# Optimization experiments

Hardware: AMD Instinct MI355X
Metric: run time of the kernel (lower is better)

The kernel has to match this reference:

```python
import jax, jax.numpy as jnp
import numpy as np
from jax import lax

B, T = 8192, 4096


def setup_inputs() -> dict:
    key = jax.random.key(0)
    kx, k1, k2, k3, k4 = jax.random.split(key, 5)
    # torch.nn.RNN default init: U(-1/sqrt(hidden), 1/sqrt(hidden)) = U(-1, 1) for hidden=1
    u = lambda k, shp: jax.random.uniform(k, shp, jnp.float32, -1.0, 1.0)
    return {
        "x": jax.random.normal(kx, (B, T, 1), jnp.float32),
        "w_ih": u(k1, (1, 1)),
        "w_hh": u(k2, (1, 1)),
        "b_ih": u(k3, (1,)),
        "b_hh": u(k4, (1,)),
    }


def reference(x, w_ih, w_hh, b_ih, b_hh):
    # Vanilla tanh RNN: h_t = tanh(x_t @ W_ih^T + b_ih + h_{t-1} @ W_hh^T + b_hh)
    # hidden=input=1, so all matmuls are scalar multiplies. Output is h at last step.
    a = w_ih[0, 0]
    b = w_hh[0, 0]
    c = b_ih[0] + b_hh[0]
    xT = jnp.swapaxes(x, 0, 1)  # [T, B, 1]

    def step(h, x_t):
        h_new = jnp.tanh(x_t * a + h * b + c)
        return h_new, None

    h0 = jnp.zeros((x.shape[0], 1), x.dtype)
    hT, _ = lax.scan(step, h0, xT)
    return hT  # [B, 1], equals rnn_output[:, -1]
```

## Files before the change

kernel.cpp:

```cpp
#include <hip/hip_runtime.h>


constexpr int T_LEN = 4096;
constexpr int NTHR  = 256;
constexpr int CH    = T_LEN / NTHR;
constexpr int NF4   = CH / 4;

typedef float fx4 __attribute__((ext_vector_type(4)));

__device__ __forceinline__ int swz(int s) { return s ^ ((s >> 2) & 7); }

#define STEP_PG(qv)                                                     \
    do {                                                                \
        float r_ = __builtin_amdgcn_rcpf(E + 1.0f);                     \
        P *= (fourb * r_) * (1.0f - r_);                                \
        E = __builtin_amdgcn_exp2f(fmaf(r_, nB4, (qv)));                \
    } while (0)

__global__ __launch_bounds__(NTHR)
void rnn_row_kernel(const float* __restrict__ x,
                    const float* __restrict__ w_ih,
                    const float* __restrict__ w_hh,
                    const float* __restrict__ b_ih,
                    const float* __restrict__ b_hh,
                    float* __restrict__ out) {
    __shared__ fx4 sm[T_LEN / 4];
    __shared__ float wP[4], wG[4];

    const int tid  = threadIdx.x;
    const int lane = tid & 63;
    const int wv   = tid >> 6;
    const int row  = blockIdx.x;

    const float a  = w_ih[0];
    const float bb = w_hh[0];
    const float cc = b_ih[0] + b_hh[0];

    const float L2E2  = 2.88539008177792681472f;
    const float A2    = a * L2E2;
    const float C2    = (bb + cc) * L2E2;
    const float nB4   = -(bb * L2E2 * 2.0f);
    const float fourb = 4.0f * bb;

    const fx4* xp = (const fx4*)(x + (size_t)row * T_LEN);
#pragma unroll
    for (int i = 0; i < 4; ++i) {
        int s = (wv << 8) + (i << 6) + lane;
        sm[swz(s)] = xp[s];
    }

    fx4 buf[NF4];
#pragma unroll
    for (int q = 0; q < NF4; ++q) buf[q] = sm[swz(tid * NF4 + q)];

    float E, P = 1.0f;
    {
        fx4 v = buf[0];
        float q0 = fmaf(v.x, A2, C2);
        float q1 = fmaf(v.y, A2, C2);
        float q2 = fmaf(v.z, A2, C2);
        float q3 = fmaf(v.w, A2, C2);
        E = __builtin_amdgcn_exp2f(fmaf(0.5f, nB4, q0));
        STEP_PG(q1); STEP_PG(q2); STEP_PG(q3);
    }
#pragma unroll
    for (int i = 1; i < NF4; ++i) {
        fx4 v = buf[i];
        float q0 = fmaf(v.x, A2, C2);
        float q1 = fmaf(v.y, A2, C2);
        float q2 = fmaf(v.z, A2, C2);
        float q3 = fmaf(v.w, A2, C2);
        STEP_PG(q0); STEP_PG(q1); STEP_PG(q2); STEP_PG(q3);
    }
    float r = __builtin_amdgcn_rcpf(E + 1.0f);
    float G = fmaf(-2.0f, r, 1.0f);
    P *= (fourb * r) * (1.0f - r);

#pragma unroll
    for (int d = 1; d < 64; d <<= 1) {
        float Pl = __shfl_up(P, d, 64);
        float Gl = __shfl_up(G, d, 64);
        if (lane >= d) {
            G = fmaf(P, Gl, G);
            P *= Pl;
        }
    }
    if (lane == 63) { wP[wv] = P; wG[wv] = G; }
    __syncthreads();

    if (tid == 0) {
        float h = wG[0];
        h = fmaf(wP[1], h, wG[1]);
        h = fmaf(wP[2], h, wG[2]);
        h = fmaf(wP[3], h, wG[3]);
        out[row] = h;
    }
}

extern "C" void kernel_launch(void* const* d_in, const int* in_sizes, int n_in,
                              void* d_out, int out_size, void* d_ws, size_t ws_size,
                              hipStream_t stream) {
    const float* x    = (const float*)d_in[0];
    const float* w_ih = (const float*)d_in[1];
    const float* w_hh = (const float*)d_in[2];
    const float* b_ih = (const float*)d_in[3];
    const float* b_hh = (const float*)d_in[4];
    float* out = (float*)d_out;

    const int B = out_size;
    dim3 grid(B), block(NTHR);
    rnn_row_kernel<<<grid, block, 0, stream>>>(x, w_ih, w_hh, b_ih, b_hh, out);
}
```

Before: 190.8 us.

## Process four rows per block with register prefetch of the next row

```diff
diff --git a/kernel.cpp b/kernel.cpp
--- a/kernel.cpp
+++ b/kernel.cpp
@@ -5,6 +5,7 @@
 constexpr int NTHR  = 256;
 constexpr int CH    = T_LEN / NTHR;
 constexpr int NF4   = CH / 4;
+constexpr int RPB   = 4;
 
 typedef float fx4 __attribute__((ext_vector_type(4)));
 
@@ -17,7 +18,7 @@
         E = __builtin_amdgcn_exp2f(fmaf(r_, nB4, (qv)));                \
     } while (0)
 
-__global__ __launch_bounds__(NTHR)
+__global__ __launch_bounds__(NTHR, 8)
 void rnn_row_kernel(const float* __restrict__ x,
                     const float* __restrict__ w_ih,
                     const float* __restrict__ w_hh,
@@ -25,12 +26,12 @@
                     const float* __restrict__ b_hh,
                     float* __restrict__ out) {
     __shared__ fx4 sm[T_LEN / 4];
-    __shared__ float wP[4], wG[4];
+    __shared__ float wP4[RPB][4], wG4[RPB][4];
 
     const int tid  = threadIdx.x;
     const int lane = tid & 63;
     const int wv   = tid >> 6;
-    const int row  = blockIdx.x;
+    const int row0 = blockIdx.x * RPB;
 
     const float a  = w_ih[0];
     const float bb = w_hh[0];
@@ -42,58 +43,79 @@
     const float nB4   = -(bb * L2E2 * 2.0f);
     const float fourb = 4.0f * bb;
 
-    const fx4* xp = (const fx4*)(x + (size_t)row * T_LEN);
+    fx4 pf[NF4];
+    {
+        const fx4* xp = (const fx4*)(x + (size_t)row0 * T_LEN);
 #pragma unroll
-    for (int i = 0; i < 4; ++i) {
-        int s = (wv << 8) + (i << 6) + lane;
-        sm[swz(s)] = xp[s];
+        for (int i = 0; i < NF4; ++i) {
+            int s = (wv << 8) + (i << 6) + lane;
+            pf[i] = __builtin_nontemporal_load(&xp[s]);
+        }
     }
 
-    fx4 buf[NF4];
 #pragma unroll
-    for (int q = 0; q < NF4; ++q) buf[q] = sm[swz(tid * NF4 + q)];
+    for (int r = 0; r < RPB; ++r) {
+#pragma unroll
+        for (int i = 0; i < NF4; ++i) {
+            int s = (wv << 8) + (i << 6) + lane;
+            sm[swz(s)] = pf[i];
+        }
+        if (r + 1 < RPB) {
+            const fx4* xn = (const fx4*)(x + (size_t)(row0 + r + 1) * T_LEN);
+#pragma unroll
+            for (int i = 0; i < NF4; ++i) {
+                int s = (wv << 8) + (i << 6) + lane;
+                pf[i] = __builtin_nontemporal_load(&xn[s]);
+            }
+        }
 
-    float E, P = 1.0f;
-    {
-        fx4 v = buf[0];
-        float q0 = fmaf(v.x, A2, C2);
-        float q1 = fmaf(v.y, A2, C2);
-        float q2 = fmaf(v.z, A2, C2);
-        float q3 = fmaf(v.w, A2, C2);
-        E = __builtin_amdgcn_exp2f(fmaf(0.5f, nB4, q0));
-        STEP_PG(q1); STEP_PG(q2); STEP_PG(q3);
-    }
+        fx4 buf[NF4];
 #pragma unroll
-    for (int i = 1; i < NF4; ++i) {
-        fx4 v = buf[i];
-        float q0 = fmaf(v.x, A2, C2);
-        float q1 = fmaf(v.y, A2, C2);
-        float q2 = fmaf(v.z, A2, C2);
-        float q3 = fmaf(v.w, A2, C2);
-        STEP_PG(q0); STEP_PG(q1); STEP_PG(q2); STEP_PG(q3);
-    }
-    float r = __builtin_amdgcn_rcpf(E + 1.0f);
-    float G = fmaf(-2.0f, r, 1.0f);
-    P *= (fourb * r) * (1.0f - r);
+        for (int q = 0; q < NF4; ++q) buf[q] = sm[swz(tid * NF4 + q)];
+
+        float E, P = 1.0f;
+        {
+            fx4 v = buf[0];
+            float q0 = fmaf(v.x, A2, C2);
+            float q1 = fmaf(v.y, A2, C2);
+            float q2 = fmaf(v.z, A2, C2);
+            float q3 = fmaf(v.w, A2, C2);
+            E = __builtin_amdgcn_exp2f(fmaf(0.5f, nB4, q0));
+            STEP_PG(q1); STEP_PG(q2); STEP_PG(q3);
+        }
+#pragma unroll
+        for (int i = 1; i < NF4; ++i) {
+            fx4 v = buf[i];
+            float q0 = fmaf(v.x, A2, C2);
+            float q1 = fmaf(v.y, A2, C2);
+            float q2 = fmaf(v.z, A2, C2);
+            float q3 = fmaf(v.w, A2, C2);
+            STEP_PG(q0); STEP_PG(q1); STEP_PG(q2); STEP_PG(q3);
+        }
+        float rr = __builtin_amdgcn_rcpf(E + 1.0f);
+        float G = fmaf(-2.0f, rr, 1.0f);
+        P *= (fourb * rr) * (1.0f - rr);
 
 #pragma unroll
-    for (int d = 1; d < 64; d <<= 1) {
-        float Pl = __shfl_up(P, d, 64);
-        float Gl = __shfl_up(G, d, 64);
-        if (lane >= d) {
-            G = fmaf(P, Gl, G);
-            P *= Pl;
+        for (int d = 1; d < 64; d <<= 1) {
+            float Pl = __shfl_up(P, d, 64);
+            float Gl = __shfl_up(G, d, 64);
+            if (lane >= d) {
+                G = fmaf(P, Gl, G);
+                P *= Pl;
+            }
         }
+        if (lane == 63) { wP4[r][wv] = P; wG4[r][wv] = G; }
     }
-    if (lane == 63) { wP[wv] = P; wG[wv] = G; }
+
     __syncthreads();
 
-    if (tid == 0) {
-        float h = wG[0];
-        h = fmaf(wP[1], h, wG[1]);
-        h = fmaf(wP[2], h, wG[2]);
-        h = fmaf(wP[3], h, wG[3]);
-        out[row] = h;
+    if (tid < RPB) {
+        float h = wG4[tid][0];
+        h = fmaf(wP4[tid][1], h, wG4[tid][1]);
+        h = fmaf(wP4[tid][2], h, wG4[tid][2]);
+        h = fmaf(wP4[tid][3], h, wG4[tid][3]);
+        out[row0 + tid] = h;
     }
 }
 
@@ -108,6 +130,6 @@
     float* out = (float*)d_out;
 
     const int B = out_size;
-    dim3 grid(B), block(NTHR);
+    dim3 grid(B / RPB), block(NTHR);
     rnn_row_kernel<<<grid, block, 0, stream>>>(x, w_ih, w_hh, b_ih, b_hh, out);
 }
```

Measured after the change: 182.3 us. -4.5%, faster.
